# Kernel optimization log

Hardware: AMD Instinct MI355X
Metric: run time of the kernel (lower is better)

The kernel has to match this reference:

```python
import jax, jax.numpy as jnp
import numpy as np

HEADS = 16
DIM_HEAD = 64
SCALE = DIM_HEAD ** -0.5
CMEM_RATIO = 4
MEM_LEN = 1024
CMEM_LEN = 256


def shift(x):
    # relative-position shift trick; x: [b, h, i, j]
    b, h, i, j = x.shape
    x = jnp.concatenate([x, jnp.zeros((b, h, i, i), x.dtype)], axis=-1)
    l = i + j - 1
    x = x.reshape(b, h, -1)
    pad = (-x.shape[-1]) % l
    x = jnp.concatenate([x, jnp.zeros((b, h, pad), x.dtype)], axis=-1).reshape(b, h, -1, l)
    return x[..., :i, i - 1:]


def setup_inputs() -> dict:
    key = jax.random.key(0)
    ks = jax.random.split(key, 8)
    b, t, e = 2, 1024, 1024
    kv_len = CMEM_LEN + MEM_LEN + t
    inp = {}
    inp['x'] = jax.random.normal(ks[0], (b, t, e), jnp.float32)
    inp['mem'] = jax.random.normal(ks[1], (b, MEM_LEN, e), jnp.float32)
    inp['cmem'] = jax.random.normal(ks[2], (b, CMEM_LEN, e), jnp.float32)
    inp['pos_emb'] = jax.random.normal(ks[3], (HEADS, kv_len, DIM_HEAD), jnp.float32)
    inp['input_mask'] = jnp.ones((b, t), bool)
    inp['Wq'] = jax.random.normal(ks[4], (e, e), jnp.float32) * 0.02
    inp['Wkv'] = jax.random.normal(ks[5], (e, 2 * e), jnp.float32) * 0.02
    inp['Wo'] = jax.random.normal(ks[6], (e, e), jnp.float32) * 0.02
    inp['bo'] = jnp.zeros((e,), jnp.float32)
    inp['conv_w'] = jax.random.normal(ks[7], (e, e, CMEM_RATIO), jnp.float32) * 0.02
    inp['conv_b'] = jnp.zeros((e,), jnp.float32)
    return inp


def _attend(x, mem, cmem, pos_emb, input_mask, Wq, Wkv):
    b, t, e = x.shape
    mem_len, cmem_len = mem.shape[1], cmem.shape[1]
    q = x @ Wq
    kv_input = jnp.concatenate([cmem, mem, x], axis=1)
    kv_len = kv_input.shape[1]
    k, v = jnp.split(kv_input @ Wkv, 2, axis=-1)
    mh = lambda z: z.reshape(b, -1, HEADS, DIM_HEAD).transpose(0, 2, 1, 3)  # [b,h,s,d]
    q, k, v = mh(q), mh(k), mh(v)
    dots = jnp.einsum('bhid,bhjd->bhij', q, k) * SCALE
    mask_value = -jnp.finfo(dots.dtype).max
    pe = pos_emb[:, -kv_len:].astype(q.dtype)
    pos_dots = jnp.einsum('bhid,hjd->bhij', q, pe) * SCALE
    dots = dots + shift(pos_dots)
    # padding mask (NOTE: replicates source: memory region is padded with False)
    pad_mask = input_mask[:, None, :, None] & input_mask[:, None, None, :]
    pad_mask = jnp.pad(pad_mask, ((0, 0), (0, 0), (0, 0), (mem_len + cmem_len, 0)), constant_values=False)
    dots = jnp.where(pad_mask, dots, mask_value)
    # causal mask exactly as in source (triu with diagonal=1+kv_len)
    causal = jnp.triu(jnp.ones((t, kv_len), bool), k=1 + kv_len)
    dots = jnp.where(causal[None, None], mask_value, dots)
    attn = jax.nn.softmax(dots, axis=-1)
    out = jnp.einsum('bhij,bhjd->bhid', attn, v)
    return out.transpose(0, 2, 1, 3).reshape(b, t, e)


def reference(x, mem, cmem, pos_emb, input_mask, Wq, Wkv, Wo, bo, conv_w, conv_b):
    b, t, e = x.shape
    out = _attend(x, mem, cmem, pos_emb, input_mask, Wq, Wkv)
    logits = out @ Wo + bo
    # memory update (eval mode, seq_len == t, calc_memory=True)
    cat_mem = jnp.concatenate([mem, x], axis=1)
    old_mem, new_mem = cat_mem[:, :-MEM_LEN], cat_mem[:, -MEM_LEN:]
    pad = old_mem.shape[1] % CMEM_RATIO
    if pad != 0:
        old_mem = jnp.pad(old_mem, ((0, 0), (pad, 0), (0, 0)))
    cm = jax.lax.conv_general_dilated(old_mem.transpose(0, 2, 1), conv_w, (CMEM_RATIO,), 'VALID',
                                      dimension_numbers=('NCH', 'OIH', 'NCH'))
    compressed = (cm + conv_b[None, :, None]).transpose(0, 2, 1)
    new_cmem = jnp.concatenate([cmem, compressed], axis=1)[:, -CMEM_LEN:]
    aux_loss = jnp.zeros((1,), x.dtype)
    return logits, new_mem, new_cmem, aux_loss
```

## Files before the change

### kernel.cpp

```cpp
#include <hip/hip_runtime.h>
#include <hip/hip_bf16.h>

typedef __bf16 bf16x8 __attribute__((ext_vector_type(8)));
typedef float f32x4 __attribute__((ext_vector_type(4)));

#define SCALE 0.125f

typedef __attribute__((address_space(1))) const unsigned int gas_u32;
typedef __attribute__((address_space(3))) unsigned int las_u32;

__device__ __forceinline__ void gload16(const void* g, void* l) {
  __builtin_amdgcn_global_load_lds((gas_u32*)g, (las_u32*)l, 16, 0, 0);
}

__device__ __forceinline__ unsigned short f2bf(float f) {
  unsigned int u = __float_as_uint(f);
  u = (u + 0x7fffu + ((u >> 16) & 1u)) >> 16;
  return (unsigned short)u;
}
__device__ __forceinline__ float bf2f(unsigned short s) {
  return __uint_as_float(((unsigned int)s) << 16);
}
__device__ __forceinline__ f32x4 f4zero() {
  f32x4 v; v[0] = 0.f; v[1] = 0.f; v[2] = 0.f; v[3] = 0.f; return v;
}
__device__ __forceinline__ bf16x8 ld8(const unsigned short* p) {
  return *(const bf16x8*)p;
}


__global__ void cast_x_mem(const float* __restrict__ x, const float* __restrict__ mem,
                           unsigned short* __restrict__ xb, unsigned short* __restrict__ memb,
                           float* __restrict__ newmem, float* __restrict__ aux) {
  long i = (long)blockIdx.x * 256 + threadIdx.x;
  if (i < 524288) {
    float4 v = ((const float4*)x)[i];
    ((float4*)newmem)[i] = v;
    ushort4 o; o.x = f2bf(v.x); o.y = f2bf(v.y); o.z = f2bf(v.z); o.w = f2bf(v.w);
    ((ushort4*)xb)[i] = o;
    if (i == 0) aux[0] = 0.f;
  } else {
    long j = i - 524288;
    float4 v = ((const float4*)mem)[j];
    ushort4 o; o.x = f2bf(v.x); o.y = f2bf(v.y); o.z = f2bf(v.z); o.w = f2bf(v.w);
    ((ushort4*)memb)[j] = o;
  }
}

__global__ void cast_pe(const float* __restrict__ pe, unsigned short* __restrict__ peb) {
  long i = (long)blockIdx.x * 256 + threadIdx.x;
  int h = (int)(i >> 14);
  int rem = (int)(i & 16383);
  const float4* src = (const float4*)(pe + ((long)h * 2304 + 1280) * 64);
  float4 v = src[rem];
  ushort4 o; o.x = f2bf(v.x); o.y = f2bf(v.y); o.z = f2bf(v.z); o.w = f2bf(v.w);
  *(ushort4*)(peb + (long)h * 65536 + (long)rem * 4) = o;
}

__global__ void transpose3(const float* __restrict__ Wq, const float* __restrict__ Wkv,
                           const float* __restrict__ Wo,
                           unsigned short* __restrict__ WbT, unsigned short* __restrict__ WoT) {
  __shared__ float tile[64][65];
  int bx = blockIdx.x;
  const float* in; unsigned short* out; int N, bxl;
  if (bx < 16)      { in = Wq;  out = WbT;           N = 1024; bxl = bx; }
  else if (bx < 48) { in = Wkv; out = WbT + 1048576; N = 2048; bxl = bx - 16; }
  else              { in = Wo;  out = WoT;           N = 1024; bxl = bx - 48; }
  int k0 = blockIdx.y * 64, n0 = bxl * 64;
  int t = threadIdx.x;
  int c = t & 63, r4 = t >> 6;
  for (int rr = r4; rr < 64; rr += 4)
    tile[rr][c] = in[(long)(k0 + rr) * N + n0 + c];
  __syncthreads();
  for (int rr = r4; rr < 64; rr += 4)
    out[(long)(n0 + rr) * 1024 + k0 + c] = f2bf(tile[c][rr]);
}

__global__ void convw_t(const float* __restrict__ cw, unsigned short* __restrict__ BcT) {
  long i = (long)blockIdx.x * 256 + threadIdx.x;
  int o = (int)(i >> 10), ii = (int)(i & 1023);
  float4 v = *(const float4*)&cw[i * 4];
  unsigned short* base = BcT + (long)o * 4096 + ii;
  base[0]    = f2bf(v.x);
  base[1024] = f2bf(v.y);
  base[2048] = f2bf(v.z);
  base[3072] = f2bf(v.w);
}

__global__ void vt_prep(const unsigned short* __restrict__ qkvb, unsigned short* __restrict__ Vt) {
  __shared__ unsigned short L[64][72];
  int tt = blockIdx.x, h = blockIdx.y, b = blockIdx.z;
  int t0 = tt * 64;
  int tid = threadIdx.x;
  int row = tid >> 2, ch = tid & 3;
  const unsigned short* src = qkvb + (long)(b * 1024 + t0 + row) * 3072 + 2048 + h * 64;
  *(uint4*)&L[row][ch * 8]       = *(const uint4*)&src[ch * 8];
  *(uint4*)&L[row][(ch + 4) * 8] = *(const uint4*)&src[(ch + 4) * 8];
  __syncthreads();
  int d = tid >> 2, tch = tid & 3;
  unsigned short* dst = Vt + ((long)((b * 16 + h) * 64 + d)) * 1024 + t0;
  for (int s = tch; s < 8; s += 4) {
    unsigned short tmp[8];
    for (int i = 0; i < 8; ++i) tmp[i] = L[s * 8 + i][d];
    *(uint4*)&dst[s * 8] = *(const uint4*)tmp;
  }
}

__global__ void splitk_reduce_bias(const float* __restrict__ part,
                                   const float* __restrict__ bias,
                                   float* __restrict__ out) {
  int i = blockIdx.x * 256 + threadIdx.x;
  float4 a = ((const float4*)part)[i];
  for (int s = 1; s < 8; ++s) {
    float4 b = ((const float4*)(part + (long)s * 524288))[i];
    a.x += b.x; a.y += b.y; a.z += b.z; a.w += b.w;
  }
  float4 bb = *(const float4*)&bias[(i * 4) & 1023];
  a.x += bb.x; a.y += bb.y; a.z += bb.z; a.w += bb.w;
  ((float4*)out)[i] = a;
}

template<int M_REP, bool OUT_F32, bool HAS_BIAS, bool SHIFT, bool SKIP>
__global__ __launch_bounds__(256) void gemm_bt(
    const unsigned short* __restrict__ A, const unsigned short* __restrict__ BT,
    void* __restrict__ Cout, const float* __restrict__ bias,
    int K, int lda, int ldbt, int ldc,
    int zInner, long sAo, long sAi, long sBo, long sBi, long sCo, long sCi) {
  if (SKIP && (int)(blockIdx.x + blockIdx.y) < 7) return;
  constexpr int BM = 32 * M_REP;
  constexpr int ACH = BM / 16;
  __shared__ unsigned short As[BM * 32];
  __shared__ unsigned short Bs[128 * 32];
  int z = blockIdx.z;
  int zo = z / zInner, zi = z % zInner;
  A += zo * sAo + zi * sAi;
  BT += zo * sBo + zi * sBi;
  long coff = zo * sCo + zi * sCi;
  int r0 = blockIdx.y * BM;
  int c0 = blockIdx.x * 128;
  int tid = threadIdx.x;
  int lane = tid & 63, wid = tid >> 6;
  int wm = wid >> 1, wn = wid & 1;
  int lr = lane & 15, lg = lane >> 4;
  int srow = lane >> 2;
  int sg8 = (((lane & 3) ^ ((lane >> 3) & 3)) * 8);

  f32x4 acc[M_REP][4];
  for (int mi = 0; mi < M_REP; ++mi)
    for (int nj = 0; nj < 4; ++nj) acc[mi][nj] = f4zero();

  int nK = K >> 5;
  for (int kt = 0; kt < nK; ++kt) {
    __syncthreads();
    for (int c = wid; c < ACH + 8; c += 4) {
      if (c < ACH) {
        int row = c * 16 + srow;
        gload16(&A[(long)(r0 + row) * lda + kt * 32 + sg8], As + c * 512);
      } else {
        int cb = c - ACH;
        int row = cb * 16 + srow;
        gload16(&BT[(long)(c0 + row) * ldbt + kt * 32 + sg8], Bs + cb * 512);
      }
    }
    __syncthreads();
    bf16x8 af[M_REP], bfr[4];
    for (int mi = 0; mi < M_REP; ++mi) {
      int row = wm * (16 * M_REP) + mi * 16 + lr;
      af[mi] = ld8(&As[row * 32 + ((lg ^ ((row >> 1) & 3)) * 8)]);
    }
    for (int nj = 0; nj < 4; ++nj) {
      int row = wn * 64 + nj * 16 + lr;
      bfr[nj] = ld8(&Bs[row * 32 + ((lg ^ ((row >> 1) & 3)) * 8)]);
    }
    for (int mi = 0; mi < M_REP; ++mi)
      for (int nj = 0; nj < 4; ++nj)
        acc[mi][nj] = __builtin_amdgcn_mfma_f32_16x16x32_bf16(af[mi], bfr[nj], acc[mi][nj], 0, 0, 0);
  }
  float* Cf = (float*)Cout;
  unsigned short* Cb = (unsigned short*)Cout;
  for (int mi = 0; mi < M_REP; ++mi)
    for (int nj = 0; nj < 4; ++nj)
      for (int j = 0; j < 4; ++j) {
        int r = r0 + wm * (16 * M_REP) + mi * 16 + lg * 4 + j;
        int c = c0 + wn * 64 + nj * 16 + lr;
        float v = acc[mi][nj][j];
        if (HAS_BIAS) v += bias[c];
        if (SHIFT) {
          int cx = c + r - 1023;
          if (cx >= 0) Cb[coff + (long)r * ldc + cx] = f2bf(v);
        } else {
          long off = coff + (long)r * ldc + c;
          if (OUT_F32) Cf[off] = v; else Cb[off] = f2bf(v);
        }
      }
}

__global__ __launch_bounds__(256) void attn_kernel(
    const unsigned short* __restrict__ qkv,
    const unsigned short* __restrict__ Vt,
    const unsigned short* __restrict__ QPs,
    unsigned short* __restrict__ obf) {
  int rt = blockIdx.x, h = blockIdx.y, b = blockIdx.z;
  int tid = threadIdx.x;
  int lane = tid & 63, w = tid >> 6;
  int lr = lane & 15, lg = lane >> 4;
  int r0 = rt * 64;

  __shared__ unsigned short Ks[64 * 64];
  __shared__ unsigned short Vs[64 * 64];
  __shared__ unsigned short Ps[4][16][72];

  bf16x8 aq0, aq1;
  {
    const unsigned short* qrow = qkv + ((long)(b * 1024 + r0 + w * 16 + lr)) * 3072 + h * 64;
    aq0 = ld8(qrow + lg * 8);
    aq1 = ld8(qrow + 32 + lg * 8);
  }
  float m[4], lsum[4];
  f32x4 acc_o[4];
  for (int j = 0; j < 4; ++j) { m[j] = -1e30f; lsum[j] = 0.f; }
  for (int n = 0; n < 4; ++n) acc_o[n] = f4zero();

  const unsigned short* kbase = qkv + (long)b * 1024 * 3072 + 1024 + h * 64;
  const unsigned short* vtb = Vt + ((long)(b * 16 + h)) * 65536;
  const unsigned short* qpb = QPs + ((long)(b * 16 + h)) * 1048576;
  int rg = r0 + w * 16 + lg * 4;

  int srow = (lane >> 3) & 7;
  int sslot = lane & 7;

  for (int kt = 0; kt < 16; ++kt) {
    int c0 = kt * 64;
    __syncthreads();
    for (int i = 0; i < 2; ++i) {
      int chunk = w * 2 + i;
      int row = chunk * 8 + srow;
      int g = sslot ^ (row & 7);
      gload16(&kbase[(long)(c0 + row) * 3072 + g * 8], Ks + chunk * 512);
      gload16(&vtb[(long)row * 1024 + c0 + g * 8], Vs + chunk * 512);
    }
    __syncthreads();
    float qpv[4][4];
    bool anyqp = (kt <= rt);
    if (anyqp) {
      for (int nj = 0; nj < 4; ++nj) {
        int cx = c0 + nj * 16 + lr;
        for (int j = 0; j < 4; ++j) {
          int r = rg + j;
          float v = bf2f(qpb[(long)r * 1024 + cx]);
          qpv[nj][j] = (kt < rt || cx <= r) ? v : 0.f;
        }
      }
    }
    f32x4 accs[4];
    for (int nj = 0; nj < 4; ++nj) {
      int row = nj * 16 + lr;
      bf16x8 bk0 = ld8(&Ks[row * 64 + ((lg ^ (row & 7)) * 8)]);
      bf16x8 bk1 = ld8(&Ks[row * 64 + (((4 + lg) ^ (row & 7)) * 8)]);
      accs[nj] = f4zero();
      accs[nj] = __builtin_amdgcn_mfma_f32_16x16x32_bf16(aq0, bk0, accs[nj], 0, 0, 0);
      accs[nj] = __builtin_amdgcn_mfma_f32_16x16x32_bf16(aq1, bk1, accs[nj], 0, 0, 0);
    }
    float sv[4][4];
    float tmax[4] = {-1e30f, -1e30f, -1e30f, -1e30f};
    for (int nj = 0; nj < 4; ++nj)
      for (int j = 0; j < 4; ++j) {
        float s = accs[nj][j];
        if (anyqp) s += qpv[nj][j];
        s *= SCALE;
        sv[nj][j] = s;
        tmax[j] = fmaxf(tmax[j], s);
      }
    for (int d = 1; d < 16; d <<= 1)
      for (int j = 0; j < 4; ++j) tmax[j] = fmaxf(tmax[j], __shfl_xor(tmax[j], d, 64));
    float sc[4], rsum[4];
    for (int j = 0; j < 4; ++j) {
      float mn = fmaxf(m[j], tmax[j]);
      sc[j] = __expf(m[j] - mn);
      m[j] = mn;
      rsum[j] = 0.f;
    }
    for (int nj = 0; nj < 4; ++nj)
      for (int j = 0; j < 4; ++j) {
        float p = __expf(sv[nj][j] - m[j]);
        rsum[j] += p;
        Ps[w][lg * 4 + j][nj * 16 + lr] = f2bf(p);
      }
    for (int d = 1; d < 16; d <<= 1)
      for (int j = 0; j < 4; ++j) rsum[j] += __shfl_xor(rsum[j], d, 64);
    for (int j = 0; j < 4; ++j) lsum[j] = lsum[j] * sc[j] + rsum[j];
    for (int n = 0; n < 4; ++n)
      for (int j = 0; j < 4; ++j) acc_o[n][j] *= sc[j];
    asm volatile("s_waitcnt lgkmcnt(0)" ::: "memory");
    __builtin_amdgcn_sched_barrier(0);
    for (int ks = 0; ks < 2; ++ks) {
      bf16x8 ap = ld8(&Ps[w][lr][ks * 32 + lg * 8]);
      for (int n = 0; n < 4; ++n) {
        int row = n * 16 + lr;
        bf16x8 bv = ld8(&Vs[row * 64 + (((ks * 4 + lg) ^ (row & 7)) * 8)]);
        acc_o[n] = __builtin_amdgcn_mfma_f32_16x16x32_bf16(ap, bv, acc_o[n], 0, 0, 0);
      }
    }
  }
  for (int n = 0; n < 4; ++n)
    for (int j = 0; j < 4; ++j) {
      float v = acc_o[n][j] / lsum[j];
      obf[((long)(b * 1024 + rg + j)) * 1024 + h * 64 + n * 16 + lr] = f2bf(v);
    }
}

extern "C" void kernel_launch(void* const* d_in, const int* in_sizes, int n_in,
                              void* d_out, int out_size, void* d_ws, size_t ws_size,
                              hipStream_t stream) {
  const float* x       = (const float*)d_in[0];
  const float* mem     = (const float*)d_in[1];
  const float* pos_emb = (const float*)d_in[3];
  const float* Wq      = (const float*)d_in[5];
  const float* Wkv     = (const float*)d_in[6];
  const float* Wo      = (const float*)d_in[7];
  const float* bo      = (const float*)d_in[8];
  const float* conv_w  = (const float*)d_in[9];
  const float* conv_b  = (const float*)d_in[10];
  float* out = (float*)d_out;

  char* ws = (char*)d_ws;
  unsigned short* xb   = (unsigned short*)(ws + 0);
  unsigned short* Vt   = xb;
  unsigned short* WbT  = (unsigned short*)(ws + 4194304);
  unsigned short* qkvb = (unsigned short*)(ws + 10485760);
  unsigned short* peb  = (unsigned short*)(ws + 23068672);
  unsigned short* obf  = (unsigned short*)(ws + 25165824);
  unsigned short* WoT  = (unsigned short*)(ws + 29360128);
  unsigned short* memb = (unsigned short*)(ws + 31457280);
  unsigned short* BcT  = (unsigned short*)(ws + 35651584);
  unsigned short* QPbf = (unsigned short*)(ws + 44040192);
  float* convpart = (float*)(ws + 44040192);

  float* logits   = out;
  float* new_mem  = out + 2097152;
  float* new_cmem = out + 4194304;
  float* aux      = out + 4718592;

  cast_x_mem<<<4096, 256, 0, stream>>>(x, mem, xb, memb, new_mem, aux);
  cast_pe<<<1024, 256, 0, stream>>>(pos_emb, peb);
  transpose3<<<dim3(64, 16), 256, 0, stream>>>(Wq, Wkv, Wo, WbT, WoT);
  convw_t<<<4096, 256, 0, stream>>>(conv_w, BcT);

  gemm_bt<2, false, false, false, false><<<dim3(24, 32, 1), 256, 0, stream>>>(
      xb, WbT, qkvb, nullptr, 1024, 1024, 1024, 3072, 1, 0, 0, 0, 0, 0, 0);

  vt_prep<<<dim3(16, 16, 2), 256, 0, stream>>>(qkvb, Vt);

  gemm_bt<4, false, false, true, true><<<dim3(8, 8, 32), 256, 0, stream>>>(
      qkvb, peb, QPbf, nullptr, 64, 3072, 64, 1024,
      16, 3145728, 64, 0, 65536, 16777216, 1048576);

  attn_kernel<<<dim3(16, 16, 2), 256, 0, stream>>>(qkvb, Vt, QPbf, obf);

  gemm_bt<2, true, true, false, false><<<dim3(8, 32, 1), 256, 0, stream>>>(
      obf, WoT, logits, bo, 1024, 1024, 1024, 1024, 1, 0, 0, 0, 0, 0, 0);

  gemm_bt<2, true, false, false, false><<<dim3(8, 8, 8), 256, 0, stream>>>(
      memb, BcT, convpart, nullptr, 512, 4096, 4096, 1024,
      1, 512, 0, 512, 0, 524288, 0);
  splitk_reduce_bias<<<512, 256, 0, stream>>>(convpart, conv_b, new_cmem);
}
```

Measured before the change: 269.9 us.

## Fuse relative-position scores into attention, double-buffer GEMM and merge prep kernels

Removes the separate Q·PE GEMM that wrote a large shifted bf16 score matrix. The attention kernel now loads position-embedding tiles into a three-slot LDS ring and computes the shifted scores in-register with MFMA plus lane shuffles. The GEMM and attention kernels gain double-buffered LDS with prefetch of the next tile, attention blocks are remapped with a swizzled block index, and the four preprocessing kernels are merged into one launch. The fusion saves a big global write and read, at the cost of more LDS, extra MFMAs and shuffles per tile, and more complex index logic that is easy to get subtly wrong.

```diff
diff --git a/kernel.cpp b/kernel.cpp
--- a/kernel.cpp
+++ b/kernel.cpp
@@ -5,6 +5,7 @@
 typedef float f32x4 __attribute__((ext_vector_type(4)));
 
 #define SCALE 0.125f
+#define MFMA16 __builtin_amdgcn_mfma_f32_16x16x32_bf16
 
 typedef __attribute__((address_space(1))) const unsigned int gas_u32;
 typedef __attribute__((address_space(3))) unsigned int las_u32;
@@ -18,9 +19,6 @@
   u = (u + 0x7fffu + ((u >> 16) & 1u)) >> 16;
   return (unsigned short)u;
 }
-__device__ __forceinline__ float bf2f(unsigned short s) {
-  return __uint_as_float(((unsigned int)s) << 16);
-}
 __device__ __forceinline__ f32x4 f4zero() {
   f32x4 v; v[0] = 0.f; v[1] = 0.f; v[2] = 0.f; v[3] = 0.f; return v;
 }
@@ -28,63 +26,64 @@
   return *(const bf16x8*)p;
 }
 
-
-__global__ void cast_x_mem(const float* __restrict__ x, const float* __restrict__ mem,
-                           unsigned short* __restrict__ xb, unsigned short* __restrict__ memb,
-                           float* __restrict__ newmem, float* __restrict__ aux) {
-  long i = (long)blockIdx.x * 256 + threadIdx.x;
-  if (i < 524288) {
-    float4 v = ((const float4*)x)[i];
-    ((float4*)newmem)[i] = v;
-    ushort4 o; o.x = f2bf(v.x); o.y = f2bf(v.y); o.z = f2bf(v.z); o.w = f2bf(v.w);
-    ((ushort4*)xb)[i] = o;
-    if (i == 0) aux[0] = 0.f;
-  } else {
-    long j = i - 524288;
-    float4 v = ((const float4*)mem)[j];
-    ushort4 o; o.x = f2bf(v.x); o.y = f2bf(v.y); o.z = f2bf(v.z); o.w = f2bf(v.w);
-    ((ushort4*)memb)[j] = o;
-  }
-}
-
-__global__ void cast_pe(const float* __restrict__ pe, unsigned short* __restrict__ peb) {
-  long i = (long)blockIdx.x * 256 + threadIdx.x;
-  int h = (int)(i >> 14);
-  int rem = (int)(i & 16383);
-  const float4* src = (const float4*)(pe + ((long)h * 2304 + 1280) * 64);
-  float4 v = src[rem];
-  ushort4 o; o.x = f2bf(v.x); o.y = f2bf(v.y); o.z = f2bf(v.z); o.w = f2bf(v.w);
-  *(ushort4*)(peb + (long)h * 65536 + (long)rem * 4) = o;
-}
-
-__global__ void transpose3(const float* __restrict__ Wq, const float* __restrict__ Wkv,
-                           const float* __restrict__ Wo,
-                           unsigned short* __restrict__ WbT, unsigned short* __restrict__ WoT) {
+__global__ void prep_all(const float* __restrict__ x, const float* __restrict__ mem,
+                         const float* __restrict__ pe,
+                         const float* __restrict__ Wq, const float* __restrict__ Wkv,
+                         const float* __restrict__ Wo, const float* __restrict__ cw,
+                         unsigned short* __restrict__ xb, unsigned short* __restrict__ memb,
+                         float* __restrict__ newmem, float* __restrict__ aux,
+                         unsigned short* __restrict__ peb,
+                         unsigned short* __restrict__ WbT, unsigned short* __restrict__ WoT,
+                         unsigned short* __restrict__ BcT) {
   __shared__ float tile[64][65];
   int bx = blockIdx.x;
-  const float* in; unsigned short* out; int N, bxl;
-  if (bx < 16)      { in = Wq;  out = WbT;           N = 1024; bxl = bx; }
-  else if (bx < 48) { in = Wkv; out = WbT + 1048576; N = 2048; bxl = bx - 16; }
-  else              { in = Wo;  out = WoT;           N = 1024; bxl = bx - 48; }
-  int k0 = blockIdx.y * 64, n0 = bxl * 64;
-  int t = threadIdx.x;
-  int c = t & 63, r4 = t >> 6;
-  for (int rr = r4; rr < 64; rr += 4)
-    tile[rr][c] = in[(long)(k0 + rr) * N + n0 + c];
-  __syncthreads();
-  for (int rr = r4; rr < 64; rr += 4)
-    out[(long)(n0 + rr) * 1024 + k0 + c] = f2bf(tile[c][rr]);
-}
-
-__global__ void convw_t(const float* __restrict__ cw, unsigned short* __restrict__ BcT) {
-  long i = (long)blockIdx.x * 256 + threadIdx.x;
-  int o = (int)(i >> 10), ii = (int)(i & 1023);
-  float4 v = *(const float4*)&cw[i * 4];
-  unsigned short* base = BcT + (long)o * 4096 + ii;
-  base[0]    = f2bf(v.x);
-  base[1024] = f2bf(v.y);
-  base[2048] = f2bf(v.z);
-  base[3072] = f2bf(v.w);
+  int tid = threadIdx.x;
+  if (bx < 4096) {
+    long i = (long)bx * 256 + tid;
+    if (i < 524288) {
+      float4 v = ((const float4*)x)[i];
+      ((float4*)newmem)[i] = v;
+      ushort4 o; o.x = f2bf(v.x); o.y = f2bf(v.y); o.z = f2bf(v.z); o.w = f2bf(v.w);
+      ((ushort4*)xb)[i] = o;
+      if (i == 0) aux[0] = 0.f;
+    } else {
+      long j = i - 524288;
+      float4 v = ((const float4*)mem)[j];
+      ushort4 o; o.x = f2bf(v.x); o.y = f2bf(v.y); o.z = f2bf(v.z); o.w = f2bf(v.w);
+      ((ushort4*)memb)[j] = o;
+    }
+  } else if (bx < 5120) {
+    long i = (long)(bx - 4096) * 256 + tid;
+    int h = (int)(i >> 14);
+    int rem = (int)(i & 16383);
+    const float4* src = (const float4*)(pe + ((long)h * 2304 + 1280) * 64);
+    float4 v = src[rem];
+    ushort4 o; o.x = f2bf(v.x); o.y = f2bf(v.y); o.z = f2bf(v.z); o.w = f2bf(v.w);
+    *(ushort4*)(peb + (long)h * 65536 + (long)rem * 4) = o;
+  } else if (bx < 9216) {
+    long i = (long)(bx - 5120) * 256 + tid;
+    int o = (int)(i >> 10), ii = (int)(i & 1023);
+    float4 v = *(const float4*)&cw[i * 4];
+    unsigned short* base = BcT + (long)o * 4096 + ii;
+    base[0]    = f2bf(v.x);
+    base[1024] = f2bf(v.y);
+    base[2048] = f2bf(v.z);
+    base[3072] = f2bf(v.w);
+  } else {
+    int t = bx - 9216;
+    int bxt = t & 63, byt = t >> 6;
+    const float* in; unsigned short* outp; int N, bxl;
+    if (bxt < 16)      { in = Wq;  outp = WbT;           N = 1024; bxl = bxt; }
+    else if (bxt < 48) { in = Wkv; outp = WbT + 1048576; N = 2048; bxl = bxt - 16; }
+    else               { in = Wo;  outp = WoT;           N = 1024; bxl = bxt - 48; }
+    int k0 = byt * 64, n0 = bxl * 64;
+    int c = tid & 63, r4 = tid >> 6;
+    for (int rr = r4; rr < 64; rr += 4)
+      tile[rr][c] = in[(long)(k0 + rr) * N + n0 + c];
+    __syncthreads();
+    for (int rr = r4; rr < 64; rr += 4)
+      outp[(long)(n0 + rr) * 1024 + k0 + c] = f2bf(tile[c][rr]);
+  }
 }
 
 __global__ void vt_prep(const unsigned short* __restrict__ qkvb, unsigned short* __restrict__ Vt) {
@@ -120,17 +119,17 @@
   ((float4*)out)[i] = a;
 }
 
-template<int M_REP, bool OUT_F32, bool HAS_BIAS, bool SHIFT, bool SKIP>
+template<int M_REP, bool OUT_F32, bool HAS_BIAS>
 __global__ __launch_bounds__(256) void gemm_bt(
     const unsigned short* __restrict__ A, const unsigned short* __restrict__ BT,
     void* __restrict__ Cout, const float* __restrict__ bias,
     int K, int lda, int ldbt, int ldc,
     int zInner, long sAo, long sAi, long sBo, long sBi, long sCo, long sCi) {
-  if (SKIP && (int)(blockIdx.x + blockIdx.y) < 7) return;
   constexpr int BM = 32 * M_REP;
   constexpr int ACH = BM / 16;
-  __shared__ unsigned short As[BM * 32];
-  __shared__ unsigned short Bs[128 * 32];
+  constexpr int ABUF = BM * 32;
+  __shared__ unsigned short As[2 * ABUF];
+  __shared__ unsigned short Bs[2 * 4096];
   int z = blockIdx.z;
   int zo = z / zInner, zi = z % zInner;
   A += zo * sAo + zi * sAi;
@@ -145,69 +144,86 @@
   int srow = lane >> 2;
   int sg8 = (((lane & 3) ^ ((lane >> 3) & 3)) * 8);
 
-  f32x4 acc[M_REP][4];
-  for (int mi = 0; mi < M_REP; ++mi)
-    for (int nj = 0; nj < 4; ++nj) acc[mi][nj] = f4zero();
-
-  int nK = K >> 5;
-  for (int kt = 0; kt < nK; ++kt) {
-    __syncthreads();
+  auto stage = [&](int kt, int buf) {
     for (int c = wid; c < ACH + 8; c += 4) {
       if (c < ACH) {
-        int row = c * 16 + srow;
-        gload16(&A[(long)(r0 + row) * lda + kt * 32 + sg8], As + c * 512);
+        gload16(&A[(long)(r0 + c * 16 + srow) * lda + kt * 32 + sg8],
+                As + buf * ABUF + c * 512);
       } else {
         int cb = c - ACH;
-        int row = cb * 16 + srow;
-        gload16(&BT[(long)(c0 + row) * ldbt + kt * 32 + sg8], Bs + cb * 512);
-      }
-    }
-    __syncthreads();
+        gload16(&BT[(long)(c0 + cb * 16 + srow) * ldbt + kt * 32 + sg8],
+                Bs + buf * 4096 + cb * 512);
+      }
+    }
+  };
+
+  f32x4 acc[M_REP][4];
+  #pragma unroll
+  for (int mi = 0; mi < M_REP; ++mi)
+    #pragma unroll
+    for (int nj = 0; nj < 4; ++nj) acc[mi][nj] = f4zero();
+
+  int nK = K >> 5;
+  stage(0, 0);
+  asm volatile("s_waitcnt vmcnt(0)" ::: "memory");
+  __syncthreads();
+  for (int kt = 0; kt < nK; ++kt) {
+    int cur = kt & 1;
+    if (kt + 1 < nK) stage(kt + 1, cur ^ 1);
     bf16x8 af[M_REP], bfr[4];
+    #pragma unroll
     for (int mi = 0; mi < M_REP; ++mi) {
       int row = wm * (16 * M_REP) + mi * 16 + lr;
-      af[mi] = ld8(&As[row * 32 + ((lg ^ ((row >> 1) & 3)) * 8)]);
-    }
+      af[mi] = ld8(&As[cur * ABUF + row * 32 + ((lg ^ ((row >> 1) & 3)) * 8)]);
+    }
+    #pragma unroll
     for (int nj = 0; nj < 4; ++nj) {
       int row = wn * 64 + nj * 16 + lr;
-      bfr[nj] = ld8(&Bs[row * 32 + ((lg ^ ((row >> 1) & 3)) * 8)]);
-    }
+      bfr[nj] = ld8(&Bs[cur * 4096 + row * 32 + ((lg ^ ((row >> 1) & 3)) * 8)]);
+    }
+    #pragma unroll
     for (int mi = 0; mi < M_REP; ++mi)
+      #pragma unroll
       for (int nj = 0; nj < 4; ++nj)
-        acc[mi][nj] = __builtin_amdgcn_mfma_f32_16x16x32_bf16(af[mi], bfr[nj], acc[mi][nj], 0, 0, 0);
+        acc[mi][nj] = MFMA16(af[mi], bfr[nj], acc[mi][nj], 0, 0, 0);
+    if (kt + 1 < nK) {
+      asm volatile("s_waitcnt vmcnt(0)" ::: "memory");
+      __syncthreads();
+    }
   }
   float* Cf = (float*)Cout;
   unsigned short* Cb = (unsigned short*)Cout;
+  #pragma unroll
   for (int mi = 0; mi < M_REP; ++mi)
+    #pragma unroll
     for (int nj = 0; nj < 4; ++nj)
+      #pragma unroll
       for (int j = 0; j < 4; ++j) {
         int r = r0 + wm * (16 * M_REP) + mi * 16 + lg * 4 + j;
         int c = c0 + wn * 64 + nj * 16 + lr;
         float v = acc[mi][nj][j];
         if (HAS_BIAS) v += bias[c];
-        if (SHIFT) {
-          int cx = c + r - 1023;
-          if (cx >= 0) Cb[coff + (long)r * ldc + cx] = f2bf(v);
-        } else {
-          long off = coff + (long)r * ldc + c;
-          if (OUT_F32) Cf[off] = v; else Cb[off] = f2bf(v);
-        }
+        long off = coff + (long)r * ldc + c;
+        if (OUT_F32) Cf[off] = v; else Cb[off] = f2bf(v);
       }
 }
 
 __global__ __launch_bounds__(256) void attn_kernel(
     const unsigned short* __restrict__ qkv,
     const unsigned short* __restrict__ Vt,
-    const unsigned short* __restrict__ QPs,
+    const unsigned short* __restrict__ peb,
     unsigned short* __restrict__ obf) {
-  int rt = blockIdx.x, h = blockIdx.y, b = blockIdx.z;
+  int bid = blockIdx.x;
+  int sw = ((bid & 7) << 6) | (bid >> 3);
+  int rt = sw & 15, h = (sw >> 4) & 15, b = sw >> 8;
   int tid = threadIdx.x;
   int lane = tid & 63, w = tid >> 6;
   int lr = lane & 15, lg = lane >> 4;
   int r0 = rt * 64;
 
-  __shared__ unsigned short Ks[64 * 64];
-  __shared__ unsigned short Vs[64 * 64];
+  __shared__ unsigned short Ks[2 * 4096];
+  __shared__ unsigned short Vs[2 * 4096];
+  __shared__ unsigned short PEs[3 * 4096];
   __shared__ unsigned short Ps[4][16][72];
 
   bf16x8 aq0, aq1;
@@ -217,92 +233,164 @@
     aq1 = ld8(qrow + 32 + lg * 8);
   }
   float m[4], lsum[4];
-  f32x4 acc_o[4];
+  f32x4 acc_o[4], accp[5];
+  #pragma unroll
   for (int j = 0; j < 4; ++j) { m[j] = -1e30f; lsum[j] = 0.f; }
+  #pragma unroll
   for (int n = 0; n < 4; ++n) acc_o[n] = f4zero();
 
-  const unsigned short* kbase = qkv + (long)b * 1024 * 3072 + 1024 + h * 64;
+  const unsigned short* kbase = qkv + (long)b * 3145728 + 1024 + h * 64;
   const unsigned short* vtb = Vt + ((long)(b * 16 + h)) * 65536;
-  const unsigned short* qpb = QPs + ((long)(b * 16 + h)) * 1048576;
+  const unsigned short* peh = peb + (long)h * 65536;
   int rg = r0 + w * 16 + lg * 4;
+  int qq = w * 16 + lg * 4;
 
   int srow = (lane >> 3) & 7;
   int sslot = lane & 7;
 
-  for (int kt = 0; kt < 16; ++kt) {
+  auto stageKV = [&](int kt, int buf) {
     int c0 = kt * 64;
-    __syncthreads();
+    #pragma unroll
     for (int i = 0; i < 2; ++i) {
       int chunk = w * 2 + i;
       int row = chunk * 8 + srow;
       int g = sslot ^ (row & 7);
-      gload16(&kbase[(long)(c0 + row) * 3072 + g * 8], Ks + chunk * 512);
-      gload16(&vtb[(long)row * 1024 + c0 + g * 8], Vs + chunk * 512);
-    }
-    __syncthreads();
-    float qpv[4][4];
-    bool anyqp = (kt <= rt);
-    if (anyqp) {
-      for (int nj = 0; nj < 4; ++nj) {
-        int cx = c0 + nj * 16 + lr;
-        for (int j = 0; j < 4; ++j) {
-          int r = rg + j;
-          float v = bf2f(qpb[(long)r * 1024 + cx]);
-          qpv[nj][j] = (kt < rt || cx <= r) ? v : 0.f;
-        }
-      }
-    }
+      gload16(&kbase[(long)(c0 + row) * 3072 + g * 8], Ks + buf * 4096 + chunk * 512);
+      gload16(&vtb[(long)row * 1024 + c0 + g * 8], Vs + buf * 4096 + chunk * 512);
+    }
+  };
+  auto stagePE = [&](int blk) {
+    int slot = blk % 3;
+    #pragma unroll
+    for (int i = 0; i < 2; ++i) {
+      int chunk = w * 2 + i;
+      int row = chunk * 8 + srow;
+      int u = min(blk * 64 + row, 1023);
+      int g = sslot ^ (row & 7);
+      gload16(&peh[(long)u * 64 + g * 8], PEs + slot * 4096 + chunk * 512);
+    }
+  };
+  auto peMFMA = [&](int pl, int ub) -> f32x4 {
+    int u = min(ub + 48 - w * 16 + pl * 16 + lr, 1023);
+    int off = ((u >> 6) % 3) * 4096 + (u & 63) * 64;
+    bf16x8 p0 = ld8(&PEs[off + ((lg ^ (u & 7)) * 8)]);
+    bf16x8 p1 = ld8(&PEs[off + (((4 + lg) ^ (u & 7)) * 8)]);
+    f32x4 r = f4zero();
+    r = MFMA16(aq0, p0, r, 0, 0, 0);
+    r = MFMA16(aq1, p1, r, 0, 0, 0);
+    return r;
+  };
+
+  stageKV(0, 0);
+  stagePE(15 - rt);
+  stagePE(16 - rt);
+  asm volatile("s_waitcnt vmcnt(0)" ::: "memory");
+  __syncthreads();
+
+  for (int kt = 0; kt < 16; ++kt) {
+    int cur = kt & 1;
+    bool band = (kt <= rt);
+    int ub = 960 + (kt - rt) * 64;
+    if (kt < 15) stageKV(kt + 1, cur ^ 1);
+    if (kt + 1 <= rt) stagePE(17 + kt - rt);
     f32x4 accs[4];
+    #pragma unroll
     for (int nj = 0; nj < 4; ++nj) {
       int row = nj * 16 + lr;
-      bf16x8 bk0 = ld8(&Ks[row * 64 + ((lg ^ (row & 7)) * 8)]);
-      bf16x8 bk1 = ld8(&Ks[row * 64 + (((4 + lg) ^ (row & 7)) * 8)]);
+      const unsigned short* kb = &Ks[cur * 4096 + row * 64];
+      bf16x8 bk0 = ld8(&kb[(lg ^ (row & 7)) * 8]);
+      bf16x8 bk1 = ld8(&kb[((4 + lg) ^ (row & 7)) * 8]);
       accs[nj] = f4zero();
-      accs[nj] = __builtin_amdgcn_mfma_f32_16x16x32_bf16(aq0, bk0, accs[nj], 0, 0, 0);
-      accs[nj] = __builtin_amdgcn_mfma_f32_16x16x32_bf16(aq1, bk1, accs[nj], 0, 0, 0);
+      accs[nj] = MFMA16(aq0, bk0, accs[nj], 0, 0, 0);
+      accs[nj] = MFMA16(aq1, bk1, accs[nj], 0, 0, 0);
+    }
+    float qpv[4][4];
+    if (band) {
+      if (kt == 0) {
+        #pragma unroll
+        for (int pl = 0; pl < 5; ++pl) accp[pl] = peMFMA(pl, ub);
+      } else {
+        #pragma unroll
+        for (int pl = 1; pl < 5; ++pl) accp[pl] = peMFMA(pl, ub);
+      }
+      #pragma unroll
+      for (int j = 0; j < 4; ++j) {
+        int sl = (lane & 48) | ((lr - lg * 4 - j - 1) & 15);
+        bool hi = lr > lg * 4 + j;
+        #pragma unroll
+        for (int nj = 0; nj < 4; ++nj) {
+          float vlo = __shfl(accp[nj][j], sl, 64);
+          float vhi = __shfl(accp[nj + 1][j], sl, 64);
+          float v = hi ? vhi : vlo;
+          if (kt == rt) {
+            int uu = nj * 16 + lr + 63 - (qq + j);
+            if (uu > 63) v = 0.f;
+          }
+          qpv[nj][j] = v;
+        }
+      }
+      accp[0] = accp[4];
     }
     float sv[4][4];
     float tmax[4] = {-1e30f, -1e30f, -1e30f, -1e30f};
+    #pragma unroll
     for (int nj = 0; nj < 4; ++nj)
+      #pragma unroll
       for (int j = 0; j < 4; ++j) {
         float s = accs[nj][j];
-        if (anyqp) s += qpv[nj][j];
+        if (band) s += qpv[nj][j];
         s *= SCALE;
         sv[nj][j] = s;
         tmax[j] = fmaxf(tmax[j], s);
       }
     for (int d = 1; d < 16; d <<= 1)
+      #pragma unroll
       for (int j = 0; j < 4; ++j) tmax[j] = fmaxf(tmax[j], __shfl_xor(tmax[j], d, 64));
     float sc[4], rsum[4];
+    #pragma unroll
     for (int j = 0; j < 4; ++j) {
       float mn = fmaxf(m[j], tmax[j]);
       sc[j] = __expf(m[j] - mn);
       m[j] = mn;
       rsum[j] = 0.f;
     }
+    #pragma unroll
     for (int nj = 0; nj < 4; ++nj)
+      #pragma unroll
       for (int j = 0; j < 4; ++j) {
         float p = __expf(sv[nj][j] - m[j]);
         rsum[j] += p;
         Ps[w][lg * 4 + j][nj * 16 + lr] = f2bf(p);
       }
     for (int d = 1; d < 16; d <<= 1)
+      #pragma unroll
       for (int j = 0; j < 4; ++j) rsum[j] += __shfl_xor(rsum[j], d, 64);
+    #pragma unroll
     for (int j = 0; j < 4; ++j) lsum[j] = lsum[j] * sc[j] + rsum[j];
+    #pragma unroll
     for (int n = 0; n < 4; ++n)
+      #pragma unroll
       for (int j = 0; j < 4; ++j) acc_o[n][j] *= sc[j];
     asm volatile("s_waitcnt lgkmcnt(0)" ::: "memory");
     __builtin_amdgcn_sched_barrier(0);
+    #pragma unroll
     for (int ks = 0; ks < 2; ++ks) {
       bf16x8 ap = ld8(&Ps[w][lr][ks * 32 + lg * 8]);
+      #pragma unroll
       for (int n = 0; n < 4; ++n) {
         int row = n * 16 + lr;
-        bf16x8 bv = ld8(&Vs[row * 64 + (((ks * 4 + lg) ^ (row & 7)) * 8)]);
-        acc_o[n] = __builtin_amdgcn_mfma_f32_16x16x32_bf16(ap, bv, acc_o[n], 0, 0, 0);
-      }
-    }
-  }
+        bf16x8 bv = ld8(&Vs[cur * 4096 + row * 64 + (((ks * 4 + lg) ^ (row & 7)) * 8)]);
+        acc_o[n] = MFMA16(ap, bv, acc_o[n], 0, 0, 0);
+      }
+    }
+    if (kt < 15) {
+      asm volatile("s_waitcnt vmcnt(0)" ::: "memory");
+      __syncthreads();
+    }
+  }
+  #pragma unroll
   for (int n = 0; n < 4; ++n)
+    #pragma unroll
     for (int j = 0; j < 4; ++j) {
       float v = acc_o[n][j] / lsum[j];
       obf[((long)(b * 1024 + rg + j)) * 1024 + h * 64 + n * 16 + lr] = f2bf(v);
@@ -333,7 +421,6 @@
   unsigned short* WoT  = (unsigned short*)(ws + 29360128);
   unsigned short* memb = (unsigned short*)(ws + 31457280);
   unsigned short* BcT  = (unsigned short*)(ws + 35651584);
-  unsigned short* QPbf = (unsigned short*)(ws + 44040192);
   float* convpart = (float*)(ws + 44040192);
 
   float* logits   = out;
@@ -341,26 +428,20 @@
   float* new_cmem = out + 4194304;
   float* aux      = out + 4718592;
 
-  cast_x_mem<<<4096, 256, 0, stream>>>(x, mem, xb, memb, new_mem, aux);
-  cast_pe<<<1024, 256, 0, stream>>>(pos_emb, peb);
-  transpose3<<<dim3(64, 16), 256, 0, stream>>>(Wq, Wkv, Wo, WbT, WoT);
-  convw_t<<<4096, 256, 0, stream>>>(conv_w, BcT);
-
-  gemm_bt<2, false, false, false, false><<<dim3(24, 32, 1), 256, 0, stream>>>(
+  prep_all<<<10240, 256, 0, stream>>>(x, mem, pos_emb, Wq, Wkv, Wo, conv_w,
+                                      xb, memb, new_mem, aux, peb, WbT, WoT, BcT);
+
+  gemm_bt<2, false, false><<<dim3(24, 32, 1), 256, 0, stream>>>(
       xb, WbT, qkvb, nullptr, 1024, 1024, 1024, 3072, 1, 0, 0, 0, 0, 0, 0);
 
   vt_prep<<<dim3(16, 16, 2), 256, 0, stream>>>(qkvb, Vt);
 
-  gemm_bt<4, false, false, true, true><<<dim3(8, 8, 32), 256, 0, stream>>>(
-      qkvb, peb, QPbf, nullptr, 64, 3072, 64, 1024,
-      16, 3145728, 64, 0, 65536, 16777216, 1048576);
-
-  attn_kernel<<<dim3(16, 16, 2), 256, 0, stream>>>(qkvb, Vt, QPbf, obf);
-
-  gemm_bt<2, true, true, false, false><<<dim3(8, 32, 1), 256, 0, stream>>>(
+  attn_kernel<<<dim3(512, 1, 1), 256, 0, stream>>>(qkvb, Vt, peb, obf);
+
+  gemm_bt<2, true, true><<<dim3(8, 32, 1), 256, 0, stream>>>(
       obf, WoT, logits, bo, 1024, 1024, 1024, 1024, 1, 0, 0, 0, 0, 0, 0);
 
-  gemm_bt<2, true, false, false, false><<<dim3(8, 8, 8), 256, 0, stream>>>(
+  gemm_bt<2, true, false><<<dim3(8, 8, 8), 256, 0, stream>>>(
       memb, BcT, convpart, nullptr, 512, 4096, 4096, 1024,
       1, 512, 0, 512, 0, 524288, 0);
   splitk_reduce_bias<<<512, 256, 0, stream>>>(convpart, conv_b, new_cmem);
```

After: 242.5 us. 1.11x faster.
